# Optimization experiments

Hardware: AMD Instinct MI355X
Metric: run time of the kernel (lower is better)

Reference implementation:

```python
import jax, jax.numpy as jnp
import numpy as np
from jax import lax

B, T, IN = 32, 512, 32
SNN, TS, HID, HOR = 128, 4, 128, 96
K = 3
THR = 1.0
EPS = 1e-5


def _spike(x):
    # heaviside: fires when (mem - threshold) > 0
    return (x > 0).astype(x.dtype)


def _lif_scan(xs, beta, thr):
    """snntorch Leaky (reset_mechanism='subtract'): mem_t = beta*mem_{t-1} + x_t - spk_{t-1}*thr; spk_t = H(mem_t - thr).
    xs: (S, B, C); beta: (C,). Returns spikes (S,B,C) and membrane (S,B,C)."""
    def step(carry, x):
        mem, rst = carry
        mem = beta * mem + x - rst * thr
        spk = _spike(mem - thr)
        return (mem, lax.stop_gradient(spk)), (spk, mem)
    z = jnp.zeros(xs.shape[1:], xs.dtype)
    _, (spks, mems) = lax.scan(step, (z, z), xs)
    return spks, mems


def setup_inputs() -> dict:
    key = jax.random.key(0)
    ks = jax.random.split(key, 10)
    def rn(k, shape, scale=0.05):
        return jax.random.normal(k, shape, dtype=jnp.float32) * scale
    return {
        "x": jax.random.normal(ks[0], (B, T, IN), dtype=jnp.float32),
        "conv_w": rn(ks[1], (SNN * TS, IN, K)),
        "conv_b": jnp.zeros((SNN * TS,), jnp.float32),
        "bn1_g": jnp.ones((SNN * TS,), jnp.float32),
        "bn1_b": jnp.zeros((SNN * TS,), jnp.float32),
        "beta1": jnp.full((SNN,), 0.9, jnp.float32),
        "bn2_g": jnp.ones((SNN,), jnp.float32),
        "bn2_b": jnp.zeros((SNN,), jnp.float32),
        "beta2": jnp.full((SNN,), 0.9, jnp.float32),
        "gru_wih": rn(ks[2], (3 * HID, IN + SNN)),
        "gru_whh": rn(ks[3], (3 * HID, HID)),
        "gru_bih": jnp.zeros((3 * HID,), jnp.float32),
        "gru_bhh": jnp.zeros((3 * HID,), jnp.float32),
        "q_w": rn(ks[4], (HID, HID)), "q_b": jnp.zeros((HID,), jnp.float32),
        "k_w": rn(ks[5], (HID, HID)), "k_b": jnp.zeros((HID,), jnp.float32),
        "v_w": rn(ks[6], (HID, HID)), "v_b": jnp.zeros((HID,), jnp.float32),
        "bn3_g": jnp.ones((HID,), jnp.float32),
        "bn3_b": jnp.zeros((HID,), jnp.float32),
        "head_w": rn(ks[7], (HOR, HID)),
        "head_b": jnp.zeros((HOR,), jnp.float32),
    }


def reference(x, conv_w, conv_b, bn1_g, bn1_b, beta1, bn2_g, bn2_b, beta2,
              gru_wih, gru_whh, gru_bih, gru_bhh, q_w, q_b, k_w, k_b, v_w, v_b,
              bn3_g, bn3_b, head_w, head_b):
    beta1 = jnp.clip(beta1, 0.0, 0.99)
    beta2 = jnp.clip(beta2, 0.0, 0.99)
    # --- ConvSpikeEncoder: Conv1d -> BatchNorm1d (training stats) -> LIF scan ---
    h = lax.conv_general_dilated(x.transpose(0, 2, 1), conv_w, (1,), [(K // 2, K // 2)],
                                 dimension_numbers=('NCH', 'OIH', 'NCH'))
    h = h + conv_b[None, :, None]  # (B, SNN*TS, T)
    m = h.mean((0, 2), keepdims=True)
    v = jnp.var(h, (0, 2), keepdims=True)
    h = (h - m) * lax.rsqrt(v + EPS) * bn1_g[None, :, None] + bn1_b[None, :, None]
    # (B, SNN*TS, T) -> (T*TS, B, SNN), step index = t*TS + s
    h = h.transpose(0, 2, 1).reshape(B, T * TS, SNN).transpose(1, 0, 2)
    spk_enc, _ = _lif_scan(h, beta1, THR)  # (T*TS, B, SNN)
    # --- per-step BatchNorm1d over batch dim, then second LIF ---
    m2 = spk_enc.mean(1, keepdims=True)
    v2 = jnp.var(spk_enc, 1, keepdims=True)
    h2 = (spk_enc - m2) * lax.rsqrt(v2 + EPS) * bn2_g + bn2_b
    _, mem_rec = _lif_scan(h2, beta2, THR)  # (T*TS, B, SNN)
    # --- downsample membrane: mean over TS sub-steps ---
    mem_down = mem_rec.transpose(1, 0, 2).reshape(B, T, TS, SNN).mean(2)  # (B, T, SNN)
    hc = jnp.concatenate([x, mem_down], -1)  # (B, T, IN+SNN)
    # --- GRU (PyTorch gate order r,z,n) ---
    def gstep(hprev, xt):
        gi = xt @ gru_wih.T + gru_bih
        gh = hprev @ gru_whh.T + gru_bhh
        ir, iz, inn = jnp.split(gi, 3, -1)
        hr, hz, hn = jnp.split(gh, 3, -1)
        r = jax.nn.sigmoid(ir + hr)
        zg = jax.nn.sigmoid(iz + hz)
        n = jnp.tanh(inn + r * hn)
        hnew = (1.0 - zg) * n + zg * hprev
        return hnew, hnew
    _, gru_seq = lax.scan(gstep, jnp.zeros((B, HID), x.dtype), hc.transpose(1, 0, 2))
    g = gru_seq.transpose(1, 0, 2)  # (B, T, HID)
    # --- SpikingAttention: sigmoid(QK^T*scale) @ V, mean over T, BatchNorm ---
    Q = g @ q_w.T + q_b
    Kk = g @ k_w.T + k_b
    V = g @ v_w.T + v_b
    attn = jax.nn.sigmoid(jnp.einsum('btc,bsc->bts', Q, Kk) * (HID ** -0.5))
    out = jnp.einsum('bts,bsc->btc', attn, V).mean(1)  # (B, HID)
    m3 = out.mean(0, keepdims=True)
    v3 = jnp.var(out, 0, keepdims=True)
    out = (out - m3) * lax.rsqrt(v3 + EPS) * bn3_g + bn3_b
    return out @ head_w.T + head_b  # (B, HOR)
```

## Files before the change

kernel.cpp:

```cpp
#include <hip/hip_runtime.h>
#include <math.h>

#define EPSV 1e-5f

#if __has_builtin(__builtin_amdgcn_exp2f)
#define EXP2F(x) __builtin_amdgcn_exp2f(x)
#else
#define EXP2F(x) exp2f(x)
#endif
#if __has_builtin(__builtin_amdgcn_rcpf)
#define RCPF(x) __builtin_amdgcn_rcpf(x)
#else
#define RCPF(x) (1.0f/(x))
#endif

__device__ __forceinline__ float fsigmoid(float x){
  return RCPF(1.0f + EXP2F(-1.4426950408889634f * x));
}
__device__ __forceinline__ float ftanh(float x){
  return RCPF(0.5f + 0.5f * EXP2F(-2.8853900817779268f * x)) - 1.0f;
}
__device__ __forceinline__ unsigned short f2bf(float f){
  unsigned u = __float_as_uint(f);
  return (unsigned short)((u + 0x7FFFu + ((u >> 16) & 1u)) >> 16);
}

typedef __attribute__((ext_vector_type(8))) short bf16x8;
typedef __attribute__((ext_vector_type(8))) short s16x8;
typedef __attribute__((ext_vector_type(4))) float f32x4;
typedef __attribute__((ext_vector_type(2))) _Float16 f16x2;
typedef __attribute__((ext_vector_type(8))) _Float16 f16x8;

#if __has_builtin(__builtin_amdgcn_fdot2)
#define FDOT2(a,b,c) __builtin_amdgcn_fdot2(a,b,c,false)
#else
__device__ __forceinline__ float FDOT2(f16x2 a, f16x2 b, float c){
  return c + (float)a[0]*(float)b[0] + (float)a[1]*(float)b[1];
}
#endif

__device__ __forceinline__ float dot8(f16x8 w, f16x8 h, float acc){
  f16x2 w0 = {w[0],w[1]}, w1 = {w[2],w[3]}, w2 = {w[4],w[5]}, w3 = {w[6],w[7]};
  f16x2 h0 = {h[0],h[1]}, h1 = {h[2],h[3]}, h2 = {h[4],h[5]}, h3 = {h[6],h[7]};
  acc = FDOT2(w0,h0,acc); acc = FDOT2(w1,h1,acc);
  acc = FDOT2(w2,h2,acc); acc = FDOT2(w3,h3,acc);
  return acc;
}

__global__ __launch_bounds__(256) void k_conv(const float* __restrict__ x, const float* __restrict__ w,
        const float* __restrict__ cb, float* __restrict__ hp, float* __restrict__ s1g, float* __restrict__ s2g,
        unsigned short* __restrict__ x_bf){
  __shared__ float xs[32*321];
  __shared__ float ws[32*97];
  __shared__ float bs[32];
  const int tid = threadIdx.x;
  const int t0 = blockIdx.x * 8;
  const int n0 = blockIdx.y * 8;
  for (int idx = tid; idx < 32*10*32; idx += 256){
    int bq = idx / 320; int rem = idx - bq*320; int tt = rem >> 5; int i = rem & 31;
    int tg = t0 - 1 + tt;
    float v = 0.f;
    if (tg >= 0 && tg < 512) v = x[(bq*512 + tg)*32 + i];
    xs[bq*321 + tt*32 + i] = v;
  }
  for (int idx = tid; idx < 32*96; idx += 256){
    int row = idx / 96; int within = idx - row*96;
    int ss = row >> 3; int nl = row & 7;
    int c = ss*128 + n0 + nl;
    ws[row*97 + within] = w[c*96 + within];
  }
  if (tid < 32){
    int ss = tid >> 3, nl = tid & 7;
    bs[tid] = cb[ss*128 + n0 + nl];
  }
  __syncthreads();
  if (blockIdx.y == 0){
    for (int idx = tid; idx < 32*8*32; idx += 256){
      int bq = idx >> 8; int rem = idx & 255; int tt = rem >> 5; int i = rem & 31;
      x_bf[(bq*512 + t0 + tt)*32 + i] = f2bf(xs[bq*321 + (tt+1)*32 + i]);
    }
  }
  const int b = tid & 31;
  const int nl = tid >> 5;
  float acc[4][8];
  #pragma unroll
  for (int ss = 0; ss < 4; ++ss){
    float bv = bs[ss*8 + nl];
    #pragma unroll
    for (int t = 0; t < 8; ++t) acc[ss][t] = bv;
  }
  for (int i = 0; i < 32; ++i){
    #pragma unroll
    for (int k = 0; k < 3; ++k){
      float w0 = ws[(0*8+nl)*97 + i*3 + k];
      float w1 = ws[(1*8+nl)*97 + i*3 + k];
      float w2 = ws[(2*8+nl)*97 + i*3 + k];
      float w3 = ws[(3*8+nl)*97 + i*3 + k];
      #pragma unroll
      for (int t = 0; t < 8; ++t){
        float xv = xs[b*321 + (t+k)*32 + i];
        acc[0][t] += xv*w0; acc[1][t] += xv*w1; acc[2][t] += xv*w2; acc[3][t] += xv*w3;
      }
    }
  }
  #pragma unroll
  for (int ss = 0; ss < 4; ++ss){
    int n = n0 + nl;
    float s1 = 0.f, s2 = 0.f;
    #pragma unroll
    for (int t = 0; t < 8; ++t){
      float v = acc[ss][t];
      int s = (t0 + t)*4 + ss;
      hp[s*4096 + n*32 + b] = v;
      s1 += v; s2 += v*v;
    }
    #pragma unroll
    for (int off = 1; off < 32; off <<= 1){
      s1 += __shfl_xor(s1, off);
      s2 += __shfl_xor(s2, off);
    }
    if (b == 0){
      int c = ss*128 + n;
      atomicAdd(&s1g[c], s1);
      atomicAdd(&s2g[c], s2);
    }
  }
}

__global__ __launch_bounds__(256) void k_cvt_all(const float* __restrict__ wih,
        const float* __restrict__ qw, const float* __restrict__ kw, const float* __restrict__ vw,
        const float* __restrict__ whh,
        unsigned short* __restrict__ wih_bf, unsigned short* __restrict__ wqkv_bf,
        _Float16* __restrict__ whh_h,
        const float* __restrict__ s1g, const float* __restrict__ s2g,
        const float* __restrict__ g, const float* __restrict__ bb,
        float* __restrict__ a1, float* __restrict__ b1){
  if (blockIdx.x >= 624){
    int c = (blockIdx.x - 624)*256 + threadIdx.x;
    if (c < 512){
      float m = s1g[c] * (1.f/16384.f);
      float v = s2g[c] * (1.f/16384.f) - m*m;
      float sc = g[c] * rsqrtf(v + EPSV);
      a1[c] = sc;
      b1[c] = bb[c] - m*sc;
    }
    return;
  }
  int i = blockIdx.x*256 + threadIdx.x;
  if (i < 61440){ wih_bf[i] = f2bf(wih[i]); return; }
  int r = i - 61440;
  if (r < 16384){ wqkv_bf[r] = f2bf(qw[r]); return; }
  r -= 16384;
  if (r < 16384){ wqkv_bf[16384 + r] = f2bf(kw[r]); return; }
  r -= 16384;
  if (r < 16384){ wqkv_bf[32768 + r] = f2bf(vw[r]); return; }
  r -= 16384;
  if (r < 49152){ whh_h[r] = (_Float16)whh[r]; }
}

__global__ __launch_bounds__(256) void k_lif(const float* __restrict__ hp,
        const float* __restrict__ a1, const float* __restrict__ b1,
        const float* __restrict__ beta1, const float* __restrict__ g2v, const float* __restrict__ b2v,
        const float* __restrict__ beta2, unsigned short* __restrict__ md_t){
  const int tid = threadIdx.x;
  const int b = tid & 31;
  const int n = blockIdx.x * 8 + (tid >> 5);
  float a1r0 = a1[0*128+n], a1r1 = a1[1*128+n], a1r2 = a1[2*128+n], a1r3 = a1[3*128+n];
  float b1r0 = b1[0*128+n], b1r1 = b1[1*128+n], b1r2 = b1[2*128+n], b1r3 = b1[3*128+n];
  float be1 = fminf(fmaxf(beta1[n], 0.f), 0.99f);
  float be2 = fminf(fmaxf(beta2[n], 0.f), 0.99f);
  float g2 = g2v[n], bb2 = b2v[n];
  float m1 = 0.f, r1 = 0.f, m2 = 0.f, r2 = 0.f;
  const float* base = hp + n*32 + b;
  float c0 = base[0], c1 = base[4096], c2 = base[2*4096], c3 = base[3*4096];
  const float* nb1 = base + 16384;
  float d0 = nb1[0], d1 = nb1[4096], d2 = nb1[2*4096], d3 = nb1[3*4096];

#define LIF_STEP(CV, A1R, B1R) { \
    float x1 = CV*A1R + B1R; \
    m1 = be1*m1 + x1 - r1; \
    bool sp = (m1 > 1.0f); \
    unsigned long long mk = __ballot(sp); \
    float spk = sp ? 1.f : 0.f; r1 = spk; \
    unsigned hf = (tid & 32) ? (unsigned)(mk >> 32) : (unsigned)mk; \
    float mean = (float)__popc(hf) * 0.03125f; \
    float var = mean - mean*mean; \
    float h2 = (spk - mean) * rsqrtf(var + EPSV) * g2 + bb2; \
    m2 = be2*m2 + h2 - r2; \
    r2 = (m2 > 1.0f) ? 1.f : 0.f; \
    accd += m2; }

  for (int t = 0; t < 512; ++t){
    float e0 = 0.f, e1 = 0.f, e2 = 0.f, e3 = 0.f;
    if (t < 510){
      const float* nb = base + (size_t)(t+2)*16384;
      e0 = nb[0]; e1 = nb[4096]; e2 = nb[2*4096]; e3 = nb[3*4096];
    }
    float accd = 0.f;
    LIF_STEP(c0, a1r0, b1r0)
    LIF_STEP(c1, a1r1, b1r1)
    LIF_STEP(c2, a1r2, b1r2)
    LIF_STEP(c3, a1r3, b1r3)
    md_t[((t*128) + n)*32 + b] = f2bf(accd * 0.25f);
    c0 = d0; c1 = d1; c2 = d2; c3 = d3;
    d0 = e0; d1 = e1; d2 = e2; d3 = e3;
  }
#undef LIF_STEP
}

__global__ __launch_bounds__(256) void k_tr(const unsigned short* __restrict__ md_t,
        unsigned short* __restrict__ md_bf){
  __shared__ unsigned short l[128][40];
  const int t = blockIdx.x;
  const int tid = threadIdx.x;
  const unsigned short* src = md_t + (size_t)t*4096;
  #pragma unroll
  for (int r = 0; r < 2; ++r){
    int idx = tid*16 + r*8;
    s16x8 v = *(const s16x8*)(src + idx);
    int nn = idx >> 5, b0 = idx & 31;
    #pragma unroll
    for (int e = 0; e < 8; ++e) l[nn][b0 + e] = (unsigned short)v[e];
  }
  __syncthreads();
  const int b = tid >> 3, seg = tid & 7;
  unsigned short tmp[16];
  #pragma unroll
  for (int i = 0; i < 16; ++i) tmp[i] = l[seg*16 + i][b];
  unsigned short* dst = md_bf + (size_t)(b*512 + t)*128 + seg*16;
  *(s16x8*)(dst + 0) = *(s16x8*)&tmp[0];
  *(s16x8*)(dst + 8) = *(s16x8*)&tmp[8];
}

__global__ __launch_bounds__(256) void k_mm_gi(const unsigned short* __restrict__ xbf,
        const unsigned short* __restrict__ mdbf, const unsigned short* __restrict__ wihbf,
        const float* __restrict__ bih, float* __restrict__ gi2){
  const int tid = threadIdx.x;
  const int w = tid >> 6, l = tid & 63;
  const int c16 = l & 15, kg = l >> 4;
  const int m0 = (blockIdx.x*4 + w) * 16;
  const int mrow = m0 + c16;
  bf16x8 a0 = *(const bf16x8*)&xbf[(size_t)mrow*32 + kg*8];
  const unsigned short* mdp = &mdbf[(size_t)mrow*128 + kg*8];
  bf16x8 a1 = *(const bf16x8*)(mdp + 0);
  bf16x8 a2 = *(const bf16x8*)(mdp + 32);
  bf16x8 a3 = *(const bf16x8*)(mdp + 64);
  bf16x8 a4 = *(const bf16x8*)(mdp + 96);
  for (int nt2 = 0; nt2 < 8; ++nt2){
    int n0 = nt2*16;
    const unsigned short* wr = &wihbf[(size_t)(      n0 + c16)*160 + kg*8];
    const unsigned short* wz = &wihbf[(size_t)(128 + n0 + c16)*160 + kg*8];
    const unsigned short* wn = &wihbf[(size_t)(256 + n0 + c16)*160 + kg*8];
    f32x4 ar = {0.f,0.f,0.f,0.f}, az = {0.f,0.f,0.f,0.f}, an = {0.f,0.f,0.f,0.f};
    #pragma unroll
    for (int c = 0; c < 5; ++c){
      bf16x8 br = *(const bf16x8*)(wr + c*32);
      bf16x8 bz = *(const bf16x8*)(wz + c*32);
      bf16x8 bn = *(const bf16x8*)(wn + c*32);
      bf16x8 aa = (c == 0) ? a0 : (c == 1) ? a1 : (c == 2) ? a2 : (c == 3) ? a3 : a4;
      ar = __builtin_amdgcn_mfma_f32_16x16x32_bf16(aa, br, ar, 0, 0, 0);
      az = __builtin_amdgcn_mfma_f32_16x16x32_bf16(aa, bz, az, 0, 0, 0);
      an = __builtin_amdgcn_mfma_f32_16x16x32_bf16(aa, bn, an, 0, 0, 0);
    }
    float br_ = bih[n0 + c16], bz_ = bih[128 + n0 + c16], bn_ = bih[256 + n0 + c16];
    int jj = n0 + c16;
    #pragma unroll
    for (int r = 0; r < 4; ++r){
      float4 o = { ar[r] + br_, az[r] + bz_, an[r] + bn_, 0.f };
      *(float4*)&gi2[(size_t)(m0 + kg*4 + r)*512 + jj*4] = o;
    }
  }
}

template<int SEL>
__device__ __forceinline__ float dpp_qp(float x){
  return __int_as_float(__builtin_amdgcn_mov_dpp(__float_as_int(x), SEL, 0xF, 0xF, true));
}
__global__ __launch_bounds__(256, 1) void k_gru(const float* __restrict__ gi2, const _Float16* __restrict__ whh_h,
        const float* __restrict__ bhh, unsigned short* __restrict__ gout_bf){
  const int b = blockIdx.x;
  const int tid = threadIdx.x;
  const int j = tid >> 1;
  const int half = tid & 1;
  const int k0 = half * 64;
  __shared__ _Float16 hs[2][144];
  const _Float16* wbr = whh_h + (size_t)(      j)*128 + k0;
  const _Float16* wbz = whh_h + (size_t)(128 + j)*128 + k0;
  const _Float16* wbn = whh_h + (size_t)(256 + j)*128 + k0;
  f16x8 wr[8], wz[8], wn[8];
  #pragma unroll
  for (int i = 0; i < 8; ++i){
    wr[i] = *(const f16x8*)(wbr + i*8);
    wz[i] = *(const f16x8*)(wbz + i*8);
    wn[i] = *(const f16x8*)(wbn + i*8);
  }
  float bh_r = 0.f, bh_z = 0.f, bh_n = 0.f;
  if (!half){
    bh_r = bhh[j]; bh_z = bhh[128+j]; bh_n = bhh[256+j];
  }
  const float* gib = gi2 + (size_t)b*512*512 + j*4;
  f32x4 G[4], N[4];
  #pragma unroll
  for (int u = 0; u < 4; ++u){
    G[u] = *(const f32x4*)(gib + (size_t)u*512);
    N[u] = *(const f32x4*)(gib + (size_t)(4+u)*512);
  }
  if (tid < 128) hs[0][tid] = (_Float16)0.f;
  float hprev = 0.f;
  __syncthreads();
  for (int g = 0; g < 128; ++g){
    f32x4 N2[4];
    if (g < 126){
      #pragma unroll
      for (int u = 0; u < 4; ++u)
        N2[u] = *(const f32x4*)(gib + (size_t)(4*(g+2)+u)*512);
    } else {
      #pragma unroll
      for (int u = 0; u < 4; ++u) N2[u] = (f32x4){0.f,0.f,0.f,0.f};
    }
    #pragma unroll
    for (int u = 0; u < 4; ++u){
      const int t = g*4 + u;
      const f16x8* hq = (const f16x8*)&hs[t & 1][k0];
      f16x8 h0 = hq[0], h1 = hq[1], h2 = hq[2], h3 = hq[3],
            h4 = hq[4], h5 = hq[5], h6 = hq[6], h7 = hq[7];
      float ar0 = 0.f, ar1 = 0.f, az0 = 0.f, az1 = 0.f, an0 = 0.f, an1 = 0.f;
      ar0 = dot8(wr[0],h0,ar0); ar0 = dot8(wr[1],h1,ar0); ar0 = dot8(wr[2],h2,ar0); ar0 = dot8(wr[3],h3,ar0);
      ar1 = dot8(wr[4],h4,ar1); ar1 = dot8(wr[5],h5,ar1); ar1 = dot8(wr[6],h6,ar1); ar1 = dot8(wr[7],h7,ar1);
      az0 = dot8(wz[0],h0,az0); az0 = dot8(wz[1],h1,az0); az0 = dot8(wz[2],h2,az0); az0 = dot8(wz[3],h3,az0);
      az1 = dot8(wz[4],h4,az1); az1 = dot8(wz[5],h5,az1); az1 = dot8(wz[6],h6,az1); az1 = dot8(wz[7],h7,az1);
      an0 = dot8(wn[0],h0,an0); an0 = dot8(wn[1],h1,an0); an0 = dot8(wn[2],h2,an0); an0 = dot8(wn[3],h3,an0);
      an1 = dot8(wn[4],h4,an1); an1 = dot8(wn[5],h5,an1); an1 = dot8(wn[6],h6,an1); an1 = dot8(wn[7],h7,an1);
      float ar = ar0 + ar1, az = az0 + az1, an = an0 + an1;
      ar += dpp_qp<0xB1>(ar);
      az += dpp_qp<0xB1>(az);
      an += dpp_qp<0xB1>(an);
      if (!half){
        float r = fsigmoid(G[u][0] + ar + bh_r);
        float z = fsigmoid(G[u][1] + az + bh_z);
        float nn = ftanh(G[u][2] + r*(an + bh_n));
        float hn = (1.f - z)*nn + z*hprev;
        hprev = hn;
        hs[(t + 1) & 1][j] = (_Float16)hn;
        gout_bf[((size_t)b*512 + t)*128 + j] = f2bf(hn);
      }
      __syncthreads();
    }
    #pragma unroll
    for (int u = 0; u < 4; ++u){ G[u] = N[u]; N[u] = N2[u]; }
  }
}

__global__ __launch_bounds__(256) void k_mm_qkv(const unsigned short* __restrict__ gbf,
        const unsigned short* __restrict__ wbf, const float* __restrict__ qb2,
        const float* __restrict__ kb2, const float* __restrict__ vb2,
        unsigned short* __restrict__ Qbf, unsigned short* __restrict__ Kbf, float* __restrict__ Vb){
  const int tid = threadIdx.x;
  const int w = tid >> 6, l = tid & 63;
  const int c16 = l & 15, kg = l >> 4;
  const int m0 = (blockIdx.x*4 + w) * 16;
  const unsigned short* gp = &gbf[(size_t)(m0 + c16)*128 + kg*8];
  bf16x8 a0 = *(const bf16x8*)(gp + 0);
  bf16x8 a1 = *(const bf16x8*)(gp + 32);
  bf16x8 a2 = *(const bf16x8*)(gp + 64);
  bf16x8 a3 = *(const bf16x8*)(gp + 96);
  for (int nt = 0; nt < 24; ++nt){
    int n0 = nt*16;
    const unsigned short* wp = &wbf[(size_t)(n0 + c16)*128 + kg*8];
    bf16x8 b0 = *(const bf16x8*)(wp + 0);
    bf16x8 b1 = *(const bf16x8*)(wp + 32);
    bf16x8 b2 = *(const bf16x8*)(wp + 64);
    bf16x8 b3 = *(const bf16x8*)(wp + 96);
    f32x4 acc = {0.f,0.f,0.f,0.f};
    acc = __builtin_amdgcn_mfma_f32_16x16x32_bf16(a0, b0, acc, 0, 0, 0);
    acc = __builtin_amdgcn_mfma_f32_16x16x32_bf16(a1, b1, acc, 0, 0, 0);
    acc = __builtin_amdgcn_mfma_f32_16x16x32_bf16(a2, b2, acc, 0, 0, 0);
    acc = __builtin_amdgcn_mfma_f32_16x16x32_bf16(a3, b3, acc, 0, 0, 0);
    int n = n0 + c16;
    if (n < 128){
      float bias = qb2[n];
      #pragma unroll
      for (int r = 0; r < 4; ++r)
        Qbf[(size_t)(m0 + kg*4 + r)*128 + n] = f2bf(acc[r] + bias);
    } else if (n < 256){
      float bias = kb2[n-128];
      #pragma unroll
      for (int r = 0; r < 4; ++r)
        Kbf[(size_t)(m0 + kg*4 + r)*128 + (n-128)] = f2bf(acc[r] + bias);
    } else {
      float bias = vb2[n-256];
      #pragma unroll
      for (int r = 0; r < 4; ++r)
        Vb[(size_t)(m0 + kg*4 + r)*128 + (n-256)] = acc[r] + bias;
    }
  }
}

__global__ __launch_bounds__(256) void k_attn(const unsigned short* __restrict__ Qbf,
        const unsigned short* __restrict__ Kbf, float* __restrict__ av){
  const int tid = threadIdx.x;
  const int b  = blockIdx.x;
  const int st = blockIdx.y;
  const int w  = tid >> 6;
  const int l  = tid & 63;
  const int c16 = l & 15;
  const int kg  = l >> 4;
  const float SC = 0.08838834764831845f;
  const unsigned short* kp = Kbf + ((size_t)(b*512 + st*64 + w*16 + c16))*128 + kg*8;
  bf16x8 a0 = *(const bf16x8*)(kp + 0);
  bf16x8 a1 = *(const bf16x8*)(kp + 32);
  bf16x8 a2 = *(const bf16x8*)(kp + 64);
  bf16x8 a3 = *(const bf16x8*)(kp + 96);
  const unsigned short* qb = Qbf + ((size_t)(b*512 + c16))*128 + kg*8;
  float ps0 = 0.f, ps1 = 0.f, ps2 = 0.f, ps3 = 0.f;
  for (int tt = 0; tt < 32; ++tt){
    const unsigned short* qp = qb + (size_t)tt*16*128;
    bf16x8 b0 = *(const bf16x8*)(qp + 0);
    bf16x8 b1 = *(const bf16x8*)(qp + 32);
    bf16x8 b2 = *(const bf16x8*)(qp + 64);
    bf16x8 b3 = *(const bf16x8*)(qp + 96);
    f32x4 acc = {0.f, 0.f, 0.f, 0.f};
    acc = __builtin_amdgcn_mfma_f32_16x16x32_bf16(a0, b0, acc, 0, 0, 0);
    acc = __builtin_amdgcn_mfma_f32_16x16x32_bf16(a1, b1, acc, 0, 0, 0);
    acc = __builtin_amdgcn_mfma_f32_16x16x32_bf16(a2, b2, acc, 0, 0, 0);
    acc = __builtin_amdgcn_mfma_f32_16x16x32_bf16(a3, b3, acc, 0, 0, 0);
    ps0 += fsigmoid(acc[0]*SC);
    ps1 += fsigmoid(acc[1]*SC);
    ps2 += fsigmoid(acc[2]*SC);
    ps3 += fsigmoid(acc[3]*SC);
  }
  #pragma unroll
  for (int off = 1; off < 16; off <<= 1){
    ps0 += __shfl_xor(ps0, off);
    ps1 += __shfl_xor(ps1, off);
    ps2 += __shfl_xor(ps2, off);
    ps3 += __shfl_xor(ps3, off);
  }
  if (c16 == 0){
    int sb = st*64 + w*16 + kg*4;
    av[b*512 + sb + 0] = ps0 * (1.f/512.f);
    av[b*512 + sb + 1] = ps1 * (1.f/512.f);
    av[b*512 + sb + 2] = ps2 * (1.f/512.f);
    av[b*512 + sb + 3] = ps3 * (1.f/512.f);
  }
}

__global__ __launch_bounds__(128) void k_av(const float* __restrict__ av, const float* __restrict__ Vb,
        float* __restrict__ out0){
  int b = blockIdx.x, c = threadIdx.x;
  float a0 = 0.f, a1 = 0.f, a2 = 0.f, a3 = 0.f;
  for (int s = 0; s < 512; s += 4){
    a0 += av[b*512 + s+0] * Vb[(size_t)(b*512 + s+0)*128 + c];
    a1 += av[b*512 + s+1] * Vb[(size_t)(b*512 + s+1)*128 + c];
    a2 += av[b*512 + s+2] * Vb[(size_t)(b*512 + s+2)*128 + c];
    a3 += av[b*512 + s+3] * Vb[(size_t)(b*512 + s+3)*128 + c];
  }
  out0[b*128 + c] = (a0 + a1) + (a2 + a3);
}

__global__ __launch_bounds__(256) void k_final(const float* __restrict__ out0,
        const float* __restrict__ g3, const float* __restrict__ b3,
        const float* __restrict__ hw, const float* __restrict__ hb, float* __restrict__ out){
  __shared__ float on[2][132];
  const int tid = threadIdx.x;
  const int b0 = blockIdx.x * 2;
  if (tid < 128){
    int c = tid;
    float s = 0.f;
    #pragma unroll 8
    for (int bq = 0; bq < 32; ++bq) s += out0[bq*128 + c];
    float m = s * (1.f/32.f);
    float v = 0.f;
    #pragma unroll 8
    for (int bq = 0; bq < 32; ++bq){ float d = out0[bq*128 + c] - m; v += d*d; }
    v *= (1.f/32.f);
    float sc = g3[c] * rsqrtf(v + EPSV);
    float sh = b3[c] - m*sc;
    on[0][c] = out0[(b0+0)*128 + c]*sc + sh;
    on[1][c] = out0[(b0+1)*128 + c]*sc + sh;
  }
  __syncthreads();
  for (int o = tid; o < 2*96; o += 256){
    int bl = o / 96, hh = o - bl*96;
    float acc = hb[hh];
    for (int k = 0; k < 128; ++k) acc += on[bl][k] * hw[hh*128 + k];
    out[(b0 + bl)*96 + hh] = acc;
  }
}

extern "C" void kernel_launch(void* const* d_in, const int* in_sizes, int n_in,
                              void* d_out, int out_size, void* d_ws, size_t ws_size,
                              hipStream_t stream){
  const float* x      = (const float*)d_in[0];
  const float* conv_w = (const float*)d_in[1];
  const float* conv_b = (const float*)d_in[2];
  const float* bn1_g  = (const float*)d_in[3];
  const float* bn1_b  = (const float*)d_in[4];
  const float* beta1  = (const float*)d_in[5];
  const float* bn2_g  = (const float*)d_in[6];
  const float* bn2_b  = (const float*)d_in[7];
  const float* beta2  = (const float*)d_in[8];
  const float* g_wih  = (const float*)d_in[9];
  const float* g_whh  = (const float*)d_in[10];
  const float* g_bih  = (const float*)d_in[11];
  const float* g_bhh  = (const float*)d_in[12];
  const float* q_w    = (const float*)d_in[13];
  const float* q_b    = (const float*)d_in[14];
  const float* k_w    = (const float*)d_in[15];
  const float* k_b    = (const float*)d_in[16];
  const float* v_w    = (const float*)d_in[17];
  const float* v_b    = (const float*)d_in[18];
  const float* bn3_g  = (const float*)d_in[19];
  const float* bn3_b  = (const float*)d_in[20];
  const float* head_w = (const float*)d_in[21];
  const float* head_b = (const float*)d_in[22];

  char* ws = (char*)d_ws;
  float* hp            = (float*)ws;
  unsigned short* md_bf= (unsigned short*)(ws + 33554432);
  unsigned short* md_t = (unsigned short*)(ws + 37748736);
  unsigned short* g_bf = (unsigned short*)(ws + 37748736);
  unsigned short* x_bf = (unsigned short*)(ws + 41943040);
  unsigned short* wih_bf  = (unsigned short*)(ws + 42991616);
  unsigned short* wqkv_bf = (unsigned short*)(ws + 43114496);
  _Float16* whh_h      = (_Float16*)(ws + 43212800);
  float* s1g = (float*)(ws + 50331648);
  float* s2g = (float*)(ws + 50331648 + 2048);
  float* a1  = (float*)(ws + 50331648 + 4096);
  float* b1  = (float*)(ws + 50331648 + 6144);
  float* av  = (float*)(ws + 50331648 + 8192);
  float* out0= (float*)(ws + 50331648 + 8192 + 65536);
  float* gi2 = (float*)ws;
  unsigned short* Qbf = (unsigned short*)ws;
  unsigned short* Kbf = (unsigned short*)(ws + 4194304);
  float* Vb  = (float*)(ws + 8388608);

  (void)hipMemsetAsync(ws + 50331648, 0, 4096, stream);

  k_conv<<<dim3(64, 16), 256, 0, stream>>>(x, conv_w, conv_b, hp, s1g, s2g, x_bf);
  k_cvt_all<<<626, 256, 0, stream>>>(g_wih, q_w, k_w, v_w, g_whh, wih_bf, wqkv_bf, whh_h,
                                     s1g, s2g, bn1_g, bn1_b, a1, b1);
  k_lif<<<16, 256, 0, stream>>>(hp, a1, b1, beta1, bn2_g, bn2_b, beta2, md_t);
  k_tr<<<512, 256, 0, stream>>>(md_t, md_bf);
  k_mm_gi<<<256, 256, 0, stream>>>(x_bf, md_bf, wih_bf, g_bih, gi2);
  k_gru<<<32, 256, 0, stream>>>(gi2, whh_h, g_bhh, g_bf);
  k_mm_qkv<<<256, 256, 0, stream>>>(g_bf, wqkv_bf, q_b, k_b, v_b, Qbf, Kbf, Vb);
  k_attn<<<dim3(32, 8), 256, 0, stream>>>(Qbf, Kbf, av);
  k_av<<<32, 128, 0, stream>>>(av, Vb, out0);
  k_final<<<16, 256, 0, stream>>>(out0, bn3_g, bn3_b, head_w, head_b, (float*)d_out);
}
```

Before: 577.4 us.

## Drop transpose kernel and spread LIF scan over more blocks

Removes the separate k_tr transpose pass. k_mm_gi now gathers its membrane operand straight from the time-major md_t buffer using strided 2-byte loads, which saves one launch and one round trip through global memory but makes the operand fetch uncoalesced. k_lif is relaunched as 64 blocks of 64 threads instead of 16 blocks of 256, so the sequential scan is spread across more compute units. The __ballot masks in the LIF step keep the same wave shape under the new block size.

```diff
diff --git a/kernel.cpp b/kernel.cpp
--- a/kernel.cpp
+++ b/kernel.cpp
@@ -48,8 +48,8 @@
 }
 
 __global__ __launch_bounds__(256) void k_conv(const float* __restrict__ x, const float* __restrict__ w,
-        const float* __restrict__ cb, float* __restrict__ hp, float* __restrict__ s1g, float* __restrict__ s2g,
-        unsigned short* __restrict__ x_bf){
+        const float* __restrict__ cb, float* __restrict__ hp, float* __restrict__ s1g,
+        float* __restrict__ s2g, unsigned short* __restrict__ x_bf){
   __shared__ float xs[32*321];
   __shared__ float ws[32*97];
   __shared__ float bs[32];
@@ -158,13 +158,13 @@
   if (r < 49152){ whh_h[r] = (_Float16)whh[r]; }
 }
 
-__global__ __launch_bounds__(256) void k_lif(const float* __restrict__ hp,
+__global__ __launch_bounds__(64) void k_lif(const float* __restrict__ hp,
         const float* __restrict__ a1, const float* __restrict__ b1,
         const float* __restrict__ beta1, const float* __restrict__ g2v, const float* __restrict__ b2v,
         const float* __restrict__ beta2, unsigned short* __restrict__ md_t){
   const int tid = threadIdx.x;
   const int b = tid & 31;
-  const int n = blockIdx.x * 8 + (tid >> 5);
+  const int n = blockIdx.x * 2 + (tid >> 5);
   float a1r0 = a1[0*128+n], a1r1 = a1[1*128+n], a1r2 = a1[2*128+n], a1r3 = a1[3*128+n];
   float b1r0 = b1[0*128+n], b1r1 = b1[1*128+n], b1r2 = b1[2*128+n], b1r3 = b1[3*128+n];
   float be1 = fminf(fmaxf(beta1[n], 0.f), 0.99f);
@@ -208,44 +208,27 @@
 #undef LIF_STEP
 }
 
-__global__ __launch_bounds__(256) void k_tr(const unsigned short* __restrict__ md_t,
-        unsigned short* __restrict__ md_bf){
-  __shared__ unsigned short l[128][40];
-  const int t = blockIdx.x;
-  const int tid = threadIdx.x;
-  const unsigned short* src = md_t + (size_t)t*4096;
-  #pragma unroll
-  for (int r = 0; r < 2; ++r){
-    int idx = tid*16 + r*8;
-    s16x8 v = *(const s16x8*)(src + idx);
-    int nn = idx >> 5, b0 = idx & 31;
-    #pragma unroll
-    for (int e = 0; e < 8; ++e) l[nn][b0 + e] = (unsigned short)v[e];
-  }
-  __syncthreads();
-  const int b = tid >> 3, seg = tid & 7;
-  unsigned short tmp[16];
-  #pragma unroll
-  for (int i = 0; i < 16; ++i) tmp[i] = l[seg*16 + i][b];
-  unsigned short* dst = md_bf + (size_t)(b*512 + t)*128 + seg*16;
-  *(s16x8*)(dst + 0) = *(s16x8*)&tmp[0];
-  *(s16x8*)(dst + 8) = *(s16x8*)&tmp[8];
-}
-
 __global__ __launch_bounds__(256) void k_mm_gi(const unsigned short* __restrict__ xbf,
-        const unsigned short* __restrict__ mdbf, const unsigned short* __restrict__ wihbf,
+        const unsigned short* __restrict__ md_t, const unsigned short* __restrict__ wihbf,
         const float* __restrict__ bih, float* __restrict__ gi2){
   const int tid = threadIdx.x;
   const int w = tid >> 6, l = tid & 63;
   const int c16 = l & 15, kg = l >> 4;
   const int m0 = (blockIdx.x*4 + w) * 16;
   const int mrow = m0 + c16;
+  const int bb = mrow >> 9, tt = mrow & 511;
   bf16x8 a0 = *(const bf16x8*)&xbf[(size_t)mrow*32 + kg*8];
-  const unsigned short* mdp = &mdbf[(size_t)mrow*128 + kg*8];
-  bf16x8 a1 = *(const bf16x8*)(mdp + 0);
-  bf16x8 a2 = *(const bf16x8*)(mdp + 32);
-  bf16x8 a3 = *(const bf16x8*)(mdp + 64);
-  bf16x8 a4 = *(const bf16x8*)(mdp + 96);
+  const unsigned short* mt = md_t + (size_t)tt*4096 + bb;
+  unsigned short tmp[4][8];
+  #pragma unroll
+  for (int f = 0; f < 4; ++f)
+    #pragma unroll
+    for (int e = 0; e < 8; ++e)
+      tmp[f][e] = mt[(kg*8 + f*32 + e)*32];
+  bf16x8 a1 = *(bf16x8*)tmp[0];
+  bf16x8 a2 = *(bf16x8*)tmp[1];
+  bf16x8 a3 = *(bf16x8*)tmp[2];
+  bf16x8 a4 = *(bf16x8*)tmp[3];
   for (int nt2 = 0; nt2 < 8; ++nt2){
     int n0 = nt2*16;
     const unsigned short* wr = &wihbf[(size_t)(      n0 + c16)*160 + kg*8];
@@ -517,7 +500,6 @@
 
   char* ws = (char*)d_ws;
   float* hp            = (float*)ws;
-  unsigned short* md_bf= (unsigned short*)(ws + 33554432);
   unsigned short* md_t = (unsigned short*)(ws + 37748736);
   unsigned short* g_bf = (unsigned short*)(ws + 37748736);
   unsigned short* x_bf = (unsigned short*)(ws + 41943040);
@@ -540,9 +522,8 @@
   k_conv<<<dim3(64, 16), 256, 0, stream>>>(x, conv_w, conv_b, hp, s1g, s2g, x_bf);
   k_cvt_all<<<626, 256, 0, stream>>>(g_wih, q_w, k_w, v_w, g_whh, wih_bf, wqkv_bf, whh_h,
                                      s1g, s2g, bn1_g, bn1_b, a1, b1);
-  k_lif<<<16, 256, 0, stream>>>(hp, a1, b1, beta1, bn2_g, bn2_b, beta2, md_t);
-  k_tr<<<512, 256, 0, stream>>>(md_t, md_bf);
-  k_mm_gi<<<256, 256, 0, stream>>>(x_bf, md_bf, wih_bf, g_bih, gi2);
+  k_lif<<<64, 64, 0, stream>>>(hp, a1, b1, beta1, bn2_g, bn2_b, beta2, md_t);
+  k_mm_gi<<<256, 256, 0, stream>>>(x_bf, md_t, wih_bf, g_bih, gi2);
   k_gru<<<32, 256, 0, stream>>>(gi2, whh_h, g_bhh, g_bf);
   k_mm_qkv<<<256, 256, 0, stream>>>(g_bf, wqkv_bf, q_b, k_b, v_b, Qbf, Kbf, Vb);
   k_attn<<<dim3(32, 8), 256, 0, stream>>>(Qbf, Kbf, av);
```

Measured after the change: 591.8 us. 1.02x slower.
